# Optimization experiments

Hardware: AMD Instinct MI355X
Metric: run time of the kernel (lower is better)

The kernel has to match this reference:

```python
import jax, jax.numpy as jnp
import numpy as np

B, S, DM, NH, L, DFF, K, VOCAB = 4, 1024, 512, 8, 6, 2048, 512, 522
DH = DM            # per-head dim equals model dim in this module (d -> n_heads*d proj)
D = NH * DH        # 4096
EPS = 1e-5


def layer_norm(x, g, b):
    m = jnp.mean(x, axis=-1, keepdims=True)
    v = jnp.var(x, axis=-1, keepdims=True)
    return (x - m) * jax.lax.rsqrt(v + EPS) * g + b


def transformer_layer(h, p):
    b, s, _ = h.shape
    q = (h @ p['Wq'] + p['bq']).reshape(b, s, NH, DH).transpose(0, 2, 1, 3)  # [b,nh,s,dh]
    k = (h @ p['Wk'] + p['bk']).reshape(b, s, NH, DH).transpose(0, 2, 1, 3)
    v = (h @ p['Wv'] + p['bv']).reshape(b, s, NH, DH).transpose(0, 2, 1, 3)
    scores = jnp.einsum('bhtd,bhsd->bhts', q, k) / np.sqrt(DH).astype(h.dtype)
    mask = jnp.triu(jnp.full((s, s), -jnp.inf, dtype=h.dtype), 1)
    scores = scores + mask
    attn = jax.nn.softmax(scores.astype(jnp.float32), axis=-1).astype(h.dtype)
    o = jnp.einsum('bhts,bhsd->bhtd', attn, v).transpose(0, 2, 1, 3).reshape(b, s, D)
    a = o @ p['Wo'] + p['bo']
    h = layer_norm(a + h, p['ln1_g'], p['ln1_b'])
    ff = jax.nn.relu(h @ p['W1'] + p['b1']) @ p['W2'] + p['b2']
    h = layer_norm(ff + h, p['ln2_g'], p['ln2_b'])
    return h


def setup_inputs() -> dict:
    key = jax.random.key(0)
    ks = iter(jax.random.split(key, 32))
    rn = lambda shape: (jax.random.normal(next(ks), shape) * 0.02).astype(jnp.float32)
    return {
        'x': jax.random.randint(next(ks), (B, S), 0, VOCAB),
        'tok_emb': rn((VOCAB, DM)),
        'pos_emb': rn((S, DM)),
        'ln_in_g': jnp.ones((DM,), jnp.float32), 'ln_in_b': jnp.zeros((DM,), jnp.float32),
        'Wq': rn((L, DM, D)), 'bq': jnp.zeros((L, D), jnp.float32),
        'Wk': rn((L, DM, D)), 'bk': jnp.zeros((L, D), jnp.float32),
        'Wv': rn((L, DM, D)), 'bv': jnp.zeros((L, D), jnp.float32),
        'Wo': rn((L, D, DM)), 'bo': jnp.zeros((L, DM), jnp.float32),
        'ln1_g': jnp.ones((L, DM), jnp.float32), 'ln1_b': jnp.zeros((L, DM), jnp.float32),
        'W1': rn((L, DM, DFF)), 'b1': jnp.zeros((L, DFF), jnp.float32),
        'W2': rn((L, DFF, DM)), 'b2': jnp.zeros((L, DM), jnp.float32),
        'ln2_g': jnp.ones((L, DM), jnp.float32), 'ln2_b': jnp.zeros((L, DM), jnp.float32),
        'W_out': rn((DM, K)), 'b_out': jnp.zeros((K,), jnp.float32),
    }


def reference(x, tok_emb, pos_emb, ln_in_g, ln_in_b, Wq, bq, Wk, bk, Wv, bv, Wo, bo,
              ln1_g, ln1_b, W1, b1, W2, b2, ln2_g, ln2_b, W_out, b_out):
    h = tok_emb[x] + pos_emb[jnp.arange(x.shape[1])][None]  # [B,S,DM]
    h = layer_norm(h, ln_in_g, ln_in_b)
    params = {'Wq': Wq, 'bq': bq, 'Wk': Wk, 'bk': bk, 'Wv': Wv, 'bv': bv,
              'Wo': Wo, 'bo': bo, 'ln1_g': ln1_g, 'ln1_b': ln1_b,
              'W1': W1, 'b1': b1, 'W2': W2, 'b2': b2, 'ln2_g': ln2_g, 'ln2_b': ln2_b}
    def body(h, p):
        return transformer_layer(h, p), None
    h, _ = jax.lax.scan(body, h, params)
    return h @ W_out + b_out  # [B,S,K]
```

## Files before the change

### kernel.cpp

```cpp
#include <hip/hip_runtime.h>
#include <math.h>


typedef unsigned short bfu;
typedef short  s16x8 __attribute__((ext_vector_type(8)));
typedef float  f32x4 __attribute__((ext_vector_type(4)));

__device__ __forceinline__ bfu f2b(float f) {
  unsigned int u = __float_as_uint(f);
  unsigned int r = (u + 0x7fffu + ((u >> 16) & 1u)) >> 16;
  return (bfu)r;
}
__device__ __forceinline__ float b2f(bfu h) {
  return __uint_as_float(((unsigned int)h) << 16);
}

__device__ __forceinline__ void async16(const bfu* g, bfu* l) {
  __builtin_amdgcn_global_load_lds(
      (const __attribute__((address_space(1))) void*)g,
      (__attribute__((address_space(3))) void*)l, 16, 0, 0);
}

template<int TM, int TN, int WY, int WX, int FI, int FJ,
         bool OUT_BF16, bool RELU, bool CAUSAL, int BIAS, bool TRIK>
__global__ __launch_bounds__(WY * WX * 64)
void gemm_bt(const bfu* __restrict__ A, long lda, long sAo, long sAi,
             const bfu* __restrict__ B, long ldb, long sBo, long sBi,
             void* __restrict__ Cv, long ldc, long sCo, long sCi,
             const float* __restrict__ bias,
             int K, int zInner, float scale, int cx)
{
  static_assert(TM == WY * FI * 16 && TN == WX * FJ * 16, "tile mismatch");
  constexpr int NW = WY * WX;
  constexpr int AI = TM / (16 * NW);
  constexpr int BI = TN / (16 * NW);
  constexpr int APAN = TM * 32;
  constexpr int BPAN = TN * 32;

  __shared__ __align__(16) bfu As[2 * APAN];
  __shared__ __align__(16) bfu Bs[2 * BPAN];

  const int NX = gridDim.x, NY = gridDim.y;
  const int flat  = blockIdx.x + NX * (blockIdx.y + NY * blockIdx.z);
  const int total = NX * NY * gridDim.z;
  const int xcd = flat & 7, idx = flat >> 3;
  const int perX = total >> 3;
  const int clX  = NX / cx;
  const int ry   = perX / cx;
  const int tx   = (xcd % clX) * cx + idx % cx;
  const int yz   = (xcd / clX) * ry + idx / cx;
  const int ty   = yz % NY, tz = yz / NY;

  const int tM = ty * TM;
  const int tN = tx * TN;
  if (CAUSAL && tN >= tM + TM) return;

  const int zo = tz / zInner, zi = tz - zo * zInner;
  A += (long)zo * sAo + (long)zi * sAi;
  B += (long)zo * sBo + (long)zi * sBi;
  const long cBase = (long)zo * sCo + (long)zi * sCi;

  const int t = threadIdx.x;
  const int wave = t >> 6, lane = t & 63;
  const int wr = wave / WX, wc = wave % WX;
  const int q = lane >> 4, l16 = lane & 15;

  const bfu* aG[AI]; bfu* aL[AI];
  const bfu* bG[BI]; bfu* bL[BI];
#pragma unroll
  for (int i2 = 0; i2 < AI; i2++) {
    const int rb = (i2 * NW + wave) * 16;
    const int r  = rb + (lane >> 2);
    const int g  = (lane & 3) ^ ((r >> 1) & 3);
    aG[i2] = A + (long)(tM + r) * lda + g * 8;
    aL[i2] = &As[rb * 32];
  }
#pragma unroll
  for (int i2 = 0; i2 < BI; i2++) {
    const int rb = (i2 * NW + wave) * 16;
    const int r  = rb + (lane >> 2);
    const int g  = (lane & 3) ^ ((r >> 1) & 3);
    bG[i2] = B + (long)(tN + r) * ldb + g * 8;
    bL[i2] = &Bs[rb * 32];
  }

  int aOff[FI], bOff[FJ];
#pragma unroll
  for (int i = 0; i < FI; i++) {
    const int r = wr * FI * 16 + i * 16 + l16;
    aOff[i] = r * 32 + ((q ^ ((r >> 1) & 3)) * 8);
  }
#pragma unroll
  for (int j = 0; j < FJ; j++) {
    const int r = wc * FJ * 16 + j * 16 + l16;
    bOff[j] = r * 32 + ((q ^ ((r >> 1) & 3)) * 8);
  }

  const int Kend = TRIK ? ((tM + TM < K) ? tM + TM : K) : K;

  f32x4 acc[FI][FJ] = {};

  for (int k0 = 0; k0 < Kend; k0 += 64) {
    __syncthreads();
#pragma unroll
    for (int m = 0; m < 2; m++) {
#pragma unroll
      for (int i2 = 0; i2 < AI; i2++) async16(aG[i2] + k0 + m * 32, aL[i2] + m * APAN);
#pragma unroll
      for (int i2 = 0; i2 < BI; i2++) async16(bG[i2] + k0 + m * 32, bL[i2] + m * BPAN);
    }
    __syncthreads();

#pragma unroll
    for (int m = 0; m < 2; m++) {
      s16x8 af[FI], bfr[FJ];
#pragma unroll
      for (int i = 0; i < FI; i++) af[i]  = *(const s16x8*)&As[m * APAN + aOff[i]];
#pragma unroll
      for (int j = 0; j < FJ; j++) bfr[j] = *(const s16x8*)&Bs[m * BPAN + bOff[j]];
#pragma unroll
      for (int i = 0; i < FI; i++)
#pragma unroll
        for (int j = 0; j < FJ; j++)
          acc[i][j] = __builtin_amdgcn_mfma_f32_16x16x32_bf16(af[i], bfr[j], acc[i][j], 0, 0, 0);
    }
  }

  float* Cf = (float*)Cv;
  bfu*   Cb = (bfu*)Cv;
#pragma unroll
  for (int i = 0; i < FI; i++) {
    const int row0 = tM + wr * FI * 16 + i * 16 + q * 4;
#pragma unroll
    for (int j = 0; j < FJ; j++) {
      const int col = tN + wc * FJ * 16 + j * 16 + l16;
      float cbv = 0.0f;
      if (BIAS == 1) cbv = bias[col];
#pragma unroll
      for (int r = 0; r < 4; r++) {
        float v = acc[i][j][r];
        if (CAUSAL) { v *= scale; if (col > row0 + r) v = -1e30f; }
        if (BIAS == 1) v += cbv;
        if (BIAS == 2) v += bias[row0 + r];
        if (RELU) v = fmaxf(v, 0.0f);
        long idxc = cBase + (long)(row0 + r) * ldc + col;
        if (OUT_BF16) Cb[idxc] = f2b(v); else Cf[idxc] = v;
      }
    }
  }
}

__global__ void transpose_cvt(const float* __restrict__ src, bfu* __restrict__ dst,
                              int R, int C)
{
  __shared__ bfu tile[64 * 65];
  const int t = threadIdx.x;
  const int tc = blockIdx.x * 64, tr = blockIdx.y * 64;
#pragma unroll
  for (int i = 0; i < 16; i++) {
    int idx = t + i * 256; int r = idx >> 6, c = idx & 63;
    tile[r * 65 + c] = f2b(src[(long)(tr + r) * C + tc + c]);
  }
  __syncthreads();
#pragma unroll
  for (int i = 0; i < 16; i++) {
    int idx = t + i * 256; int r = idx >> 6, c = idx & 63;
    dst[(long)(tc + r) * R + tr + c] = tile[c * 65 + r];
  }
}

__global__ void prep_layer(const float* __restrict__ Wq, const float* __restrict__ Wk,
                           const float* __restrict__ Wv, const float* __restrict__ Wo,
                           const float* __restrict__ W1, const float* __restrict__ W2,
                           const float* __restrict__ bq, const float* __restrict__ bk,
                           bfu* __restrict__ qkvwT, bfu* __restrict__ woT,
                           bfu* __restrict__ w1T, bfu* __restrict__ w2T,
                           float* __restrict__ qkb)
{
  const int bid = blockIdx.x;
  const int t = threadIdx.x;

  if (bid >= 2560) {
    int j = (bid - 2560) * 256 + t;
    qkb[j] = (j < 4096) ? bq[j] : bk[j - 4096];
    return;
  }

  const float* src; bfu* dst; int R, C, ctiles, local;
  if (bid < 512)       { src = Wq; dst = qkvwT;              R = 512;  C = 4096; ctiles = 64; local = bid; }
  else if (bid < 1024) { src = Wk; dst = qkvwT + 4096L*512;  R = 512;  C = 4096; ctiles = 64; local = bid - 512; }
  else if (bid < 1536) { src = Wv; dst = qkvwT + 8192L*512;  R = 512;  C = 4096; ctiles = 64; local = bid - 1024; }
  else if (bid < 2048) { src = Wo; dst = woT;                R = 4096; C = 512;  ctiles = 8;  local = bid - 1536; }
  else if (bid < 2304) { src = W1; dst = w1T;                R = 512;  C = 2048; ctiles = 32; local = bid - 2048; }
  else                 { src = W2; dst = w2T;                R = 2048; C = 512;  ctiles = 8;  local = bid - 2304; }
  const int tc = (local % ctiles) * 64;
  const int tr = (local / ctiles) * 64;

  __shared__ bfu tile[64 * 65];
#pragma unroll
  for (int i = 0; i < 16; i++) {
    int idx = t + i * 256; int r = idx >> 6, c = idx & 63;
    tile[r * 65 + c] = f2b(src[(long)(tr + r) * C + tc + c]);
  }
  __syncthreads();
#pragma unroll
  for (int i = 0; i < 16; i++) {
    int idx = t + i * 256; int r = idx >> 6, c = idx & 63;
    dst[(long)(tc + r) * R + tr + c] = tile[c * 65 + r];
  }
}

__device__ __forceinline__ void blk_stats(float s, float ss, float* red,
                                          float& mean, float& var)
{
#pragma unroll
  for (int off = 32; off; off >>= 1) { s += __shfl_down(s, off); ss += __shfl_down(ss, off); }
  int w = threadIdx.x >> 6;
  if ((threadIdx.x & 63) == 0) { red[w] = s; red[4 + w] = ss; }
  __syncthreads();
  s  = red[0] + red[1] + red[2] + red[3];
  ss = red[4] + red[5] + red[6] + red[7];
  mean = s * (1.0f / 512.0f);
  var  = ss * (1.0f / 512.0f) - mean * mean;
}

__global__ void embed_ln(const int* __restrict__ ids, const float* __restrict__ tok,
                         const float* __restrict__ pos, const float* __restrict__ g,
                         const float* __restrict__ bta, float* __restrict__ h,
                         bfu* __restrict__ hb)
{
  __shared__ float red[8];
  const int row = blockIdx.x;
  const int s = row & 1023;
  const int t = threadIdx.x;
  const long base = (long)row * 512;
  const int id = ids[row];
  float x0 = tok[(long)id * 512 + t]       + pos[(long)s * 512 + t];
  float x1 = tok[(long)id * 512 + t + 256] + pos[(long)s * 512 + t + 256];
  float mean, var;
  blk_stats(x0 + x1, x0 * x0 + x1 * x1, red, mean, var);
  float rstd = rsqrtf(var + 1e-5f);
  float y0 = (x0 - mean) * rstd * g[t]       + bta[t];
  float y1 = (x1 - mean) * rstd * g[t + 256] + bta[t + 256];
  h[base + t] = y0;        h[base + t + 256] = y1;
  hb[base + t] = f2b(y0);  hb[base + t + 256] = f2b(y1);
}

__global__ void add_ln_redN(const float* __restrict__ p, long ps, int n,
                            const float* __restrict__ bias,
                            float* __restrict__ h, bfu* __restrict__ hb,
                            const float* __restrict__ g, const float* __restrict__ bta)
{
  __shared__ float red[8];
  const long base = (long)blockIdx.x * 512;
  const int t = threadIdx.x;
  float x0 = bias[t]       + h[base + t];
  float x1 = bias[t + 256] + h[base + t + 256];
  for (int s = 0; s < n; s++) {
    x0 += p[base + (long)s * ps + t];
    x1 += p[base + (long)s * ps + t + 256];
  }
  float mean, var;
  blk_stats(x0 + x1, x0 * x0 + x1 * x1, red, mean, var);
  float rstd = rsqrtf(var + 1e-5f);
  float y0 = (x0 - mean) * rstd * g[t]       + bta[t];
  float y1 = (x1 - mean) * rstd * g[t + 256] + bta[t + 256];
  h[base + t] = y0;        h[base + t + 256] = y1;
  hb[base + t] = f2b(y0);  hb[base + t + 256] = f2b(y1);
}

__global__ void out_redN(const float* __restrict__ p, long ps, int n,
                         const float* __restrict__ bias, float* __restrict__ out)
{
  const long base = (long)blockIdx.x * 512;
  const int t = threadIdx.x;
  float x0 = bias[t], x1 = bias[t + 256];
  for (int s = 0; s < n; s++) {
    x0 += p[base + (long)s * ps + t];
    x1 += p[base + (long)s * ps + t + 256];
  }
  out[base + t] = x0;
  out[base + t + 256] = x1;
}

__global__ void softmax_causal(bfu* __restrict__ P)
{
  __shared__ float red[8];
  const long base = (long)blockIdx.x * 1024;
  const int r = blockIdx.x & 1023;
  const int wlim = ((r >> 7) + 1) << 7;
  const int t = threadIdx.x;
  float v[4];
  float mx = -3e30f;
#pragma unroll
  for (int i = 0; i < 4; i++) {
    const int col = t + i * 256;
    v[i] = (col <= r) ? b2f(P[base + col]) : -3e30f;
    mx = fmaxf(mx, v[i]);
  }
#pragma unroll
  for (int off = 32; off; off >>= 1) mx = fmaxf(mx, __shfl_xor(mx, off));
  int w = t >> 6;
  if ((t & 63) == 0) red[w] = mx;
  __syncthreads();
  mx = fmaxf(fmaxf(red[0], red[1]), fmaxf(red[2], red[3]));
  float e[4], sum = 0.0f;
#pragma unroll
  for (int i = 0; i < 4; i++) {
    const int col = t + i * 256;
    e[i] = (col <= r) ? expf(v[i] - mx) : 0.0f;
    sum += e[i];
  }
#pragma unroll
  for (int off = 32; off; off >>= 1) sum += __shfl_xor(sum, off);
  __syncthreads();
  if ((t & 63) == 0) red[4 + w] = sum;
  __syncthreads();
  sum = red[4] + red[5] + red[6] + red[7];
  float inv = 1.0f / sum;
#pragma unroll
  for (int i = 0; i < 4; i++) {
    const int col = t + i * 256;
    if (col < wlim) P[base + col] = f2b(e[i] * inv);
  }
}

extern "C" void kernel_launch(void* const* d_in, const int* in_sizes, int n_in,
                              void* d_out, int out_size, void* d_ws, size_t ws_size,
                              hipStream_t stream)
{
  const int*   x     = (const int*)  d_in[0];
  const float* tok   = (const float*)d_in[1];
  const float* pos   = (const float*)d_in[2];
  const float* lnig  = (const float*)d_in[3];
  const float* lnib  = (const float*)d_in[4];
  const float* Wq    = (const float*)d_in[5];
  const float* bq    = (const float*)d_in[6];
  const float* Wk    = (const float*)d_in[7];
  const float* bk    = (const float*)d_in[8];
  const float* Wv    = (const float*)d_in[9];
  const float* bv    = (const float*)d_in[10];
  const float* Wo    = (const float*)d_in[11];
  const float* bo    = (const float*)d_in[12];
  const float* ln1g  = (const float*)d_in[13];
  const float* ln1b  = (const float*)d_in[14];
  const float* W1    = (const float*)d_in[15];
  const float* b1    = (const float*)d_in[16];
  const float* W2    = (const float*)d_in[17];
  const float* b2    = (const float*)d_in[18];
  const float* ln2g  = (const float*)d_in[19];
  const float* ln2b  = (const float*)d_in[20];
  const float* Wout  = (const float*)d_in[21];
  const float* bout  = (const float*)d_in[22];

  const size_t MB = 1024 * 1024;
  int gb; bool s4;
  if      (ws_size >= 236 * MB) { gb = 4; s4 = true;  }
  else if (ws_size >= 169 * MB) { gb = 2; s4 = true;  }
  else if (ws_size >= 152 * MB) { gb = 1; s4 = true;  }
  else                          { gb = 1; s4 = false; }

  const size_t qkBytes = (size_t)gb * 1024 * 8192 * 2;
  const size_t scB0    = (size_t)gb * 8 * 1024 * 1024 * 2;
  const size_t scBytes = s4 ? (scB0 > 33554432 ? scB0 : 33554432) : 16777216;
  const size_t vtB0    = (size_t)gb * 8 * 512 * 1024 * 2;
  const size_t vtBytes = s4 ? (vtB0 > 33554432 ? vtB0 : 33554432) : 8388608;

  char* wsp = (char*)d_ws;
  auto alloc = [&](size_t bytes) { char* p = wsp; wsp += (bytes + 255) & ~(size_t)255; return p; };

  bfu*   qkvwT = (bfu*)  alloc(12288L * 512 * 2);
  bfu*   woT   = (bfu*)  alloc(512L * 4096 * 2);
  bfu*   w1T   = (bfu*)  alloc(2048L * 512 * 2);
  bfu*   w2T   = (bfu*)  alloc(512L * 2048 * 2);
  bfu*   woutT = (bfu*)  alloc(512L * 512 * 2);
  float* qkb   = (float*)alloc(8192L * 4);
  float* h     = (float*)alloc(4096L * 512 * 4);
  bfu*   hb    = (bfu*)  alloc(4096L * 512 * 2);
  bfu*   attn  = (bfu*)  alloc(4096L * 4096 * 2);
  bfu*   qkS   = (bfu*)  alloc(qkBytes);
  bfu*   scS   = (bfu*)  alloc(scBytes);
  bfu*   vTS   = (bfu*)  alloc(vtBytes);

  float* pWo = (float*)scS;
  float* pF  = s4 ? (float*)vTS : (float*)qkS;
  const int nspl = s4 ? 4 : 2;

  embed_ln<<<4096, 256, 0, stream>>>(x, tok, pos, lnig, lnib, h, hb);
  transpose_cvt<<<dim3(8, 8), 256, 0, stream>>>(Wout, woutT, 512, 512);

  const float invsq = 0.044194173824159216f;
  const long  PSTR  = 4096L * 512;

  for (int l = 0; l < 6; l++) {
    prep_layer<<<2592, 256, 0, stream>>>(
        Wq + (long)l*512*4096, Wk + (long)l*512*4096, Wv + (long)l*512*4096,
        Wo + (long)l*4096*512, W1 + (long)l*512*2048, W2 + (long)l*2048*512,
        bq + (long)l*4096, bk + (long)l*4096,
        qkvwT, woT, w1T, w2T, qkb);

    for (int g0 = 0; g0 < 4; g0 += gb) {
      const bfu* hbG = hb + (long)g0 * 1024 * 512;

      gemm_bt<128,128,2,2,4,4,true,false,false,1,false>
          <<<dim3(64, gb*8, 1), 256, 0, stream>>>(
          hbG, 512, 0, 0, qkvwT, 512, 0, 0, qkS, 8192, 0, 0,
          qkb, 512, 1, 1.0f, 8);

      gemm_bt<128,128,2,2,4,4,true,false,false,2,false>
          <<<dim3(8, 32, gb), 256, 0, stream>>>(
          qkvwT + 8192L*512, 512, 0, 0,
          hbG, 512, 0, 1024L*512,
          vTS, 1024, 0, 4096L*1024,
          bv + (long)l*4096, 512, gb, 1.0f, 8);

      gemm_bt<128,128,2,2,4,4,true,false,true,0,false>
          <<<dim3(8, 8, gb*8), 256, 0, stream>>>(
          qkS,        8192, 1024L*8192, 512,
          qkS + 4096, 8192, 1024L*8192, 512,
          scS, 1024, 8L*1024*1024, 1024L*1024,
          nullptr, 512, 8, invsq, 8);

      softmax_causal<<<gb*8192, 256, 0, stream>>>(scS);

      gemm_bt<128,64,2,2,4,2,true,false,false,0,true>
          <<<dim3(8, 8, gb*8), 256, 0, stream>>>(
          scS, 1024, 8L*1024*1024, 1024L*1024,
          vTS, 1024, 8L*512*1024,  512L*1024,
          attn + (long)g0*1024*4096, 4096, 1024L*4096, 512,
          nullptr, 1024, 8, 1.0f, 8);
    }

    if (s4) {
      gemm_bt<128,128,2,2,4,4,false,false,false,0,false>
          <<<dim3(4, 32, 4), 256, 0, stream>>>(
          attn, 4096, 0, 1024, woT, 4096, 0, 1024,
          pWo, 512, 0, PSTR, nullptr, 1024, 4, 1.0f, 4);
    } else {
      gemm_bt<128,64,2,2,4,2,false,false,false,0,false>
          <<<dim3(8, 32, 2), 256, 0, stream>>>(
          attn, 4096, 0, 2048, woT, 4096, 0, 2048,
          pWo, 512, 0, PSTR, nullptr, 2048, 1, 1.0f, 8);
    }
    add_ln_redN<<<4096, 256, 0, stream>>>(pWo, PSTR, nspl, bo + (long)l*512,
                                          h, hb, ln1g + (long)l*512, ln1b + (long)l*512);

    gemm_bt<128,128,2,2,4,4,true,true,false,1,false>
        <<<dim3(16, 32, 1), 256, 0, stream>>>(
        hb, 512, 0, 0, w1T, 512, 0, 0, scS, 2048, 0, 0,
        b1 + (long)l*2048, 512, 1, 1.0f, 16);

    if (s4) {
      gemm_bt<128,128,2,2,4,4,false,false,false,0,false>
          <<<dim3(4, 32, 4), 256, 0, stream>>>(
          scS, 2048, 0, 512, w2T, 2048, 0, 512,
          pF, 512, 0, PSTR, nullptr, 512, 4, 1.0f, 4);
    } else {
      gemm_bt<128,64,2,2,4,2,false,false,false,0,false>
          <<<dim3(8, 32, 2), 256, 0, stream>>>(
          scS, 2048, 0, 1024, w2T, 2048, 0, 1024,
          pF, 512, 0, PSTR, nullptr, 1024, 1, 1.0f, 8);
    }
    add_ln_redN<<<4096, 256, 0, stream>>>(pF, PSTR, nspl, b2 + (long)l*512,
                                          h, hb, ln2g + (long)l*512, ln2b + (long)l*512);
  }

  if (s4) {
    gemm_bt<128,128,2,2,4,4,false,false,false,0,false>
        <<<dim3(4, 32, 4), 256, 0, stream>>>(
        hb, 512, 0, 128, woutT, 512, 0, 128,
        pF, 512, 0, PSTR, nullptr, 128, 4, 1.0f, 4);
  } else {
    gemm_bt<128,64,2,2,4,2,false,false,false,0,false>
        <<<dim3(8, 32, 2), 256, 0, stream>>>(
        hb, 512, 0, 256, woutT, 512, 0, 256,
        pF, 512, 0, PSTR, nullptr, 256, 1, 1.0f, 8);
  }
  out_redN<<<4096, 256, 0, stream>>>(pF, PSTR, nspl, bout, (float*)d_out);
}
```

Before: 1.992 ms.

## Triple-buffer GEMM K-loop with async LDS loads and vmcnt-based waits

Replaces the load-all-then-compute double-panel GEMM loop with a 3-stage ring of 32-wide K panels. Loads for step t+2 are issued before computing step t, and s_waitcnt vmcnt waits only for the current panel. Raw s_barrier replaces __syncthreads, and s_setprio raises priority around the MFMA block. The aim is to overlap global-to-LDS transfer latency with MFMA work, at the cost of more shared memory (lower occupancy) and fragile vmcnt counting.

```diff
diff --git a/kernel.cpp b/kernel.cpp
--- a/kernel.cpp
+++ b/kernel.cpp
@@ -19,6 +19,15 @@
   __builtin_amdgcn_global_load_lds(
       (const __attribute__((address_space(1))) void*)g,
       (__attribute__((address_space(3))) void*)l, 16, 0, 0);
+}
+
+template<int N> __device__ __forceinline__ void waitvm() {
+  static_assert(N == 0 || N == 3 || N == 4 || N == 6 || N == 8, "vmcnt imm");
+  if constexpr      (N == 0) asm volatile("s_waitcnt vmcnt(0)" ::: "memory");
+  else if constexpr (N == 3) asm volatile("s_waitcnt vmcnt(3)" ::: "memory");
+  else if constexpr (N == 4) asm volatile("s_waitcnt vmcnt(4)" ::: "memory");
+  else if constexpr (N == 6) asm volatile("s_waitcnt vmcnt(6)" ::: "memory");
+  else                       asm volatile("s_waitcnt vmcnt(8)" ::: "memory");
 }
 
 template<int TM, int TN, int WY, int WX, int FI, int FJ,
@@ -34,11 +43,12 @@
   constexpr int NW = WY * WX;
   constexpr int AI = TM / (16 * NW);
   constexpr int BI = TN / (16 * NW);
+  constexpr int LP = AI + BI;
   constexpr int APAN = TM * 32;
   constexpr int BPAN = TN * 32;
 
-  __shared__ __align__(16) bfu As[2 * APAN];
-  __shared__ __align__(16) bfu Bs[2 * BPAN];
+  __shared__ __align__(16) bfu As[3 * APAN];
+  __shared__ __align__(16) bfu Bs[3 * BPAN];
 
   const int NX = gridDim.x, NY = gridDim.y;
   const int flat  = blockIdx.x + NX * (blockIdx.y + NY * blockIdx.z);
@@ -97,33 +107,45 @@
   }
 
   const int Kend = TRIK ? ((tM + TM < K) ? tM + TM : K) : K;
+  const int nt   = Kend >> 5;
+
+  auto stage = [&](int pan, int k) {
+#pragma unroll
+    for (int i2 = 0; i2 < AI; i2++) async16(aG[i2] + k, aL[i2] + pan * APAN);
+#pragma unroll
+    for (int i2 = 0; i2 < BI; i2++) async16(bG[i2] + k, bL[i2] + pan * BPAN);
+  };
 
   f32x4 acc[FI][FJ] = {};
 
-  for (int k0 = 0; k0 < Kend; k0 += 64) {
-    __syncthreads();
-#pragma unroll
-    for (int m = 0; m < 2; m++) {
-#pragma unroll
-      for (int i2 = 0; i2 < AI; i2++) async16(aG[i2] + k0 + m * 32, aL[i2] + m * APAN);
-#pragma unroll
-      for (int i2 = 0; i2 < BI; i2++) async16(bG[i2] + k0 + m * 32, bL[i2] + m * BPAN);
-    }
-    __syncthreads();
-
-#pragma unroll
-    for (int m = 0; m < 2; m++) {
-      s16x8 af[FI], bfr[FJ];
-#pragma unroll
-      for (int i = 0; i < FI; i++) af[i]  = *(const s16x8*)&As[m * APAN + aOff[i]];
-#pragma unroll
-      for (int j = 0; j < FJ; j++) bfr[j] = *(const s16x8*)&Bs[m * BPAN + bOff[j]];
-#pragma unroll
-      for (int i = 0; i < FI; i++)
-#pragma unroll
-        for (int j = 0; j < FJ; j++)
-          acc[i][j] = __builtin_amdgcn_mfma_f32_16x16x32_bf16(af[i], bfr[j], acc[i][j], 0, 0, 0);
-    }
+  stage(0, 0);
+  if (nt > 1) stage(1, 32);
+
+  int pc = 0, ps = 2;
+  for (int tt = 0; tt < nt; ++tt) {
+    if (tt + 2 < nt) { stage(ps, (tt + 2) * 32); waitvm<2 * LP>(); }
+    else if (tt + 1 < nt) waitvm<LP>();
+    else waitvm<0>();
+    __builtin_amdgcn_s_barrier();
+    __builtin_amdgcn_sched_barrier(0);
+
+    s16x8 af[FI], bfr[FJ];
+#pragma unroll
+    for (int i = 0; i < FI; i++) af[i]  = *(const s16x8*)&As[pc * APAN + aOff[i]];
+#pragma unroll
+    for (int j = 0; j < FJ; j++) bfr[j] = *(const s16x8*)&Bs[pc * BPAN + bOff[j]];
+
+    __builtin_amdgcn_s_setprio(1);
+#pragma unroll
+    for (int i = 0; i < FI; i++)
+#pragma unroll
+      for (int j = 0; j < FJ; j++)
+        acc[i][j] = __builtin_amdgcn_mfma_f32_16x16x32_bf16(af[i], bfr[j], acc[i][j], 0, 0, 0);
+    __builtin_amdgcn_s_setprio(0);
+
+    __builtin_amdgcn_s_barrier();
+    pc = (pc == 2) ? 0 : pc + 1;
+    ps = (ps == 2) ? 0 : ps + 1;
   }
 
   float* Cf = (float*)Cv;
```

After: 1.961 ms. About the same (-1.6%).
